# Kernel optimization log

Measured on AMD Instinct MI355X. Metric: run time of the kernel, lower is better.

The kernel has to match this reference:

```python
import jax, jax.numpy as jnp
import numpy as np

BACKBONE_C = 480
NUM_SEG = 4
HIDDEN = 128
IN_DIM = 2 + BACKBONE_C + NUM_SEG + 2  # 488
N_NODES = 200000
N_EDGES = 800000
FH = FW = 128


def _bilinear_sample(feat, vertices, image_size):
    # feat: (C, H, W); vertices: (N, 2) in pixel space.
    # Matches F.grid_sample(..., mode='bilinear', align_corners=True) with
    # grid = vertices/image_size*2 - 1  =>  ix = vx/image_size*(W-1).
    C, H, W = feat.shape
    ix = vertices[:, 0] / image_size * (W - 1)
    iy = vertices[:, 1] / image_size * (H - 1)
    x0 = jnp.floor(ix)
    y0 = jnp.floor(iy)
    wx = ix - x0
    wy = iy - y0
    x0i = jnp.clip(x0.astype(jnp.int32), 0, W - 1)
    x1i = jnp.clip(x0i + 1, 0, W - 1)
    y0i = jnp.clip(y0.astype(jnp.int32), 0, H - 1)
    y1i = jnp.clip(y0i + 1, 0, H - 1)
    f00 = feat[:, y0i, x0i]  # (C, N)
    f01 = feat[:, y0i, x1i]
    f10 = feat[:, y1i, x0i]
    f11 = feat[:, y1i, x1i]
    out = (f00 * (1 - wx) * (1 - wy) + f01 * wx * (1 - wy)
           + f10 * (1 - wx) * wy + f11 * wx * wy)
    return out.T  # (N, C)


def setup_inputs() -> dict:
    key = jax.random.key(0)
    k = jax.random.split(key, 8)
    vertices = jax.random.uniform(k[0], (N_NODES, 2), jnp.float32) * 512.0
    backbone_features = jax.random.normal(k[1], (1, BACKBONE_C, FH, FW), jnp.float32)
    seg_probs = jax.random.uniform(k[2], (1, NUM_SEG, FH, FW), jnp.float32)
    edge_index = jax.random.randint(k[3], (2, N_EDGES), 0, N_NODES, jnp.int64)
    s1 = 1.0 / np.sqrt(IN_DIM)
    s2 = 1.0 / np.sqrt(HIDDEN)
    W1 = jax.random.uniform(k[4], (HIDDEN, IN_DIM), jnp.float32, -s1, s1)
    b1 = jax.random.uniform(k[5], (HIDDEN,), jnp.float32, -s1, s1)
    W2 = jax.random.uniform(k[6], (HIDDEN, HIDDEN), jnp.float32, -s2, s2)
    b2 = jax.random.uniform(k[7], (HIDDEN,), jnp.float32, -s2, s2)
    return {"vertices": vertices, "backbone_features": backbone_features,
            "seg_probs": seg_probs, "edge_index": edge_index,
            "W1": W1, "b1": b1, "W2": W2, "b2": b2, "image_size": 512}


def reference(vertices, backbone_features, seg_probs, edge_index, W1, b1, W2, b2, image_size):
    N = vertices.shape[0]
    coords_norm = vertices / image_size  # (N, 2)
    backbone_feats = _bilinear_sample(backbone_features[0], vertices, image_size)  # (N, C)
    seg_stats = _bilinear_sample(seg_probs[0], vertices, image_size)  # (N, num_seg)
    # degree via scatter-add over both endpoints
    idx = jnp.concatenate([edge_index[0], edge_index[1]]).astype(jnp.int32)
    degree = jax.ops.segment_sum(jnp.ones(idx.shape[0], jnp.float32), idx, num_segments=N)
    degree_norm = degree / (degree.max() + 1e-6)
    # distance to nearest image boundary, normalized by image_size/2
    dx = jnp.minimum(vertices[:, 0], image_size - vertices[:, 0])
    dy = jnp.minimum(vertices[:, 1], image_size - vertices[:, 1])
    dist_to_boundary = jnp.minimum(dx, dy) / (image_size / 2)
    structural = jnp.stack([degree_norm, dist_to_boundary], axis=1)  # (N, 2)
    node_feats = jnp.concatenate([coords_norm, backbone_feats, seg_stats, structural], axis=1)  # (N, 488)
    h = jax.nn.relu(node_feats @ W1.T + b1)
    h = jax.nn.relu(h @ W2.T + b2)
    return h
```

## Files before the change

kernel.cpp:

```cpp
#include <hip/hip_runtime.h>

typedef _Float16 half_t;
typedef __attribute__((ext_vector_type(2))) _Float16 halfx2;
typedef __attribute__((ext_vector_type(8))) _Float16 halfx8;
typedef __attribute__((ext_vector_type(4))) float floatx4;

#define N_NODES 200000
#define N_EDGES 800000
#define NPOS    16384
#define KIN     484

#define NSLICE  32
#define NRANGE  8
#define RNODES  25000
#define RWORDS  6250
#define CWORDS  50000
#define SCHUNK  12500

#define WS_DEGPK 0
#define WS_DEG   6400000
#define WS_MAXD  7200000
#define WS_W1C   7200064
#define WS_W2F   7202112
#define WS_W1F   7234880
#define WS_U     7365952

__global__ __launch_bounds__(256) void k0(const float* __restrict__ W1,
                                          const float* __restrict__ W2,
                                          half_t* __restrict__ w2f,
                                          half_t* __restrict__ w1f,
                                          float4* __restrict__ w1c,
                                          unsigned* __restrict__ maxd) {
  const int tid = threadIdx.x, bid = blockIdx.x;
  const int wave = tid >> 6, lane = tid & 63;
  const int l15 = lane & 15, q4 = lane >> 4;

  if (bid == 0) {
    if (tid == 0) *maxd = 0u;
    if (tid < 128) {
      const float* row = W1 + tid * 488;
      w1c[tid] = make_float4(row[0], row[1], row[486], row[487]);
    }
    for (int i = tid; i < 128 * 128; i += 256) {
      int k8   = i & 7;
      int il15 = (i >> 3) & 15;
      int iq4  = (i >> 7) & 3;
      int ks32 = (i >> 9) & 1;
      int hh   = (i >> 10) & 1;
      int t    = i >> 11;
      int row = t * 16 + il15;
      int col = hh * 64 + ks32 * 32 + iq4 * 8 + k8;
      w2f[i] = (half_t)W2[row * 128 + col];
    }
  } else {
    const int t = bid - 1;
    const int j = t * 16 + l15;
    for (int c = 0; c < 4; ++c) {
      int kbi = c * 4 + wave;
      halfx8 h;
      for (int i = 0; i < 8; ++i) {
        int k = kbi * 32 + q4 * 8 + i;
        h[i] = (half_t)((k < KIN) ? W1[j * 488 + 2 + k] : 0.f);
      }
      *(halfx8*)&w1f[(t * 16 + kbi) * 512 + lane * 8] = h;
    }
  }
}

__global__ __launch_bounds__(256) void k1(const float* __restrict__ bb,
                                          const float* __restrict__ seg,
                                          const int* __restrict__ e,
                                          const half_t* __restrict__ w1f,
                                          unsigned* __restrict__ degpk,
                                          half_t* __restrict__ U) {
  __shared__ __align__(16) char sm[25600];

  const int tid = threadIdx.x, bid = blockIdx.x;
  const int wave = tid >> 6, lane = tid & 63;

  if (bid < 256) {
    const int l15 = lane & 15, q4 = lane >> 4;
    const int kk = lane >> 1, ph = lane & 1;
    const int n0 = bid * 64;
    half_t* Ol = (half_t*)sm;
    half_t* Bp = (half_t*)(sm + 17408) + wave * 640;
    const int pbase = n0 + wave * 16 + ph * 8;

    floatx4 acc[8];
    for (int t = 0; t < 8; ++t) acc[t] = (floatx4){0.f, 0.f, 0.f, 0.f};

    for (int kbi = 0; kbi < 16; ++kbi) {
      const int k = kbi * 32 + kk;
      float vals[8];
      if (k < 480) {
        const float* src = bb + (long)k * NPOS + pbase;
        float4 a = *(const float4*)src;
        float4 b4 = *(const float4*)(src + 4);
        vals[0] = a.x; vals[1] = a.y; vals[2] = a.z; vals[3] = a.w;
        vals[4] = b4.x; vals[5] = b4.y; vals[6] = b4.z; vals[7] = b4.w;
      } else if (k < KIN) {
        const float* src = seg + (long)(k - 480) * NPOS + pbase;
        float4 a = *(const float4*)src;
        float4 b4 = *(const float4*)(src + 4);
        vals[0] = a.x; vals[1] = a.y; vals[2] = a.z; vals[3] = a.w;
        vals[4] = b4.x; vals[5] = b4.y; vals[6] = b4.z; vals[7] = b4.w;
      } else {
        for (int i = 0; i < 8; ++i) vals[i] = 0.f;
      }
      for (int i = 0; i < 8; ++i)
        Bp[(ph * 8 + i) * 40 + kk] = (half_t)vals[i];

      halfx8 af = *(const halfx8*)&Bp[l15 * 40 + q4 * 8];
      for (int t = 0; t < 8; ++t) {
        halfx8 bf = *(const halfx8*)&w1f[(t * 16 + kbi) * 512 + lane * 8];
        acc[t] = __builtin_amdgcn_mfma_f32_16x16x32_f16(af, bf, acc[t], 0, 0, 0);
      }
    }

    for (int t = 0; t < 8; ++t)
      for (int r = 0; r < 4; ++r)
        Ol[(wave * 16 + q4 * 4 + r) * 136 + t * 16 + l15] = (half_t)acc[t][r];
    __syncthreads();
    for (int it = 0; it < 4; ++it) {
      int idx = tid + it * 256;
      int n = idx >> 4, c8 = (idx & 15) * 8;
      *(halfx8*)(U + (long)(n0 + n) * 128 + c8) = *(const halfx8*)&Ol[n * 136 + c8];
    }
  } else {
    unsigned* cnt = (unsigned*)sm;
    const int hb = bid - 256;
    const int s  = hb >> 3;
    const int r  = hb & 7;
    const int lo = r * RNODES;

    for (int i = tid; i < 64 + RWORDS; i += 256) cnt[i] = 0;
    __syncthreads();

#define HBIN(v) { unsigned d = (unsigned)(v) - (unsigned)lo;                 \
                  bool ok = d < (unsigned)RNODES;                            \
                  unsigned w = ok ? (d >> 2) + 64u : (unsigned)lane;         \
                  unsigned a_ = ok ? (1u << ((d & 3u) << 3)) : 0u;           \
                  atomicAdd(&cnt[w], a_); }

    const int4* E4 = (const int4*)e + s * SCHUNK;
    for (int base = 0; base < 12288; base += 1024) {
      int4 a = E4[base + tid];
      int4 b = E4[base + tid + 256];
      int4 c = E4[base + tid + 512];
      int4 d4 = E4[base + tid + 768];
      HBIN(a.x); HBIN(a.y); HBIN(a.z); HBIN(a.w);
      HBIN(b.x); HBIN(b.y); HBIN(b.z); HBIN(b.w);
      HBIN(c.x); HBIN(c.y); HBIN(c.z); HBIN(c.w);
      HBIN(d4.x); HBIN(d4.y); HBIN(d4.z); HBIN(d4.w);
    }
    if (tid < SCHUNK - 12288) {
      int4 a = E4[12288 + tid];
      HBIN(a.x); HBIN(a.y); HBIN(a.z); HBIN(a.w);
    }
#undef HBIN
    __syncthreads();

    unsigned* dst = degpk + s * CWORDS + r * RWORDS;
    for (int i = tid; i < RWORDS; i += 256) dst[i] = cnt[64 + i];
  }
}

__global__ __launch_bounds__(256) void k2(const unsigned* __restrict__ degpk,
                                          unsigned* __restrict__ deg,
                                          unsigned* __restrict__ maxd) {
  const int w4 = blockIdx.x * 256 + threadIdx.x;
  unsigned m = 0;
  if (w4 < CWORDS / 4) {
    uint4 s = make_uint4(0u, 0u, 0u, 0u);
    for (int c = 0; c < NSLICE; ++c) {
      uint4 v = *(const uint4*)&degpk[c * CWORDS + w4 * 4];
      s.x += v.x; s.y += v.y; s.z += v.z; s.w += v.w;
    }
    unsigned words[4] = {s.x, s.y, s.z, s.w};
    for (int k = 0; k < 4; ++k) {
      unsigned sw = words[k];
      uint4 o = make_uint4(sw & 255u, (sw >> 8) & 255u,
                           (sw >> 16) & 255u, sw >> 24);
      *(uint4*)&deg[w4 * 16 + k * 4] = o;
      m = max(m, max(max(o.x, o.y), max(o.z, o.w)));
    }
  }
  for (int off = 32; off > 0; off >>= 1) {
    unsigned o = (unsigned)__shfl_down((int)m, off);
    m = max(m, o);
  }
  if ((threadIdx.x & 63) == 0) atomicMax(maxd, m);
}

__global__ __launch_bounds__(256, 8) void k_main(const float* __restrict__ vertices,
                                              const float4* __restrict__ w1c,
                                              const float* __restrict__ b1,
                                              const float* __restrict__ b2,
                                              const unsigned* __restrict__ deg,
                                              const unsigned* __restrict__ maxd,
                                              const half_t* __restrict__ U,
                                              const half_t* __restrict__ w2f,
                                              float* __restrict__ out) {
  __shared__ half_t At[64 * 136];
  __shared__ int   pPos[64];
  __shared__ float pW[4][64];
  __shared__ float pE[4][64];
  __shared__ float b2l[128];

  const int tid = threadIdx.x;
  const int nodeBase = blockIdx.x * 64;

  if (tid < 128) b2l[tid] = b2[tid];

  if (tid < 64) {
    int n = nodeBase + tid;
    float vx = vertices[2 * n], vy = vertices[2 * n + 1];
    float ix = vx * (127.0f / 512.0f), iy = vy * (127.0f / 512.0f);
    float fx = floorf(ix), fy = floorf(iy);
    float wx = ix - fx, wy = iy - fy;
    int x0 = min(max((int)fx, 0), 127);
    int y0 = min(max((int)fy, 0), 127);
    pPos[tid] = y0 * 128 + x0;
    pW[0][tid] = (1.f - wx) * (1.f - wy);
    pW[1][tid] = wx * (1.f - wy);
    pW[2][tid] = (1.f - wx) * wy;
    pW[3][tid] = wx * wy;
    pE[0][tid] = vx * (1.f / 512.f);
    pE[1][tid] = vy * (1.f / 512.f);
    float md = (float)(*maxd) + 1e-6f;
    pE[2][tid] = (float)deg[n] / md;
    float dx = fminf(vx, 512.f - vx), dy = fminf(vy, 512.f - vy);
    pE[3][tid] = fminf(dx, dy) * (1.f / 256.f);
  }

  const int jp = tid & 63, q = tid >> 6;
  const int j2 = jp * 2;
  float4 cA = w1c[j2], cB = w1c[j2 + 1];
  float c00 = cA.x, c01 = cA.y, c06 = cA.z, c07 = cA.w;
  float c10 = cB.x, c11 = cB.y, c16 = cB.z, c17 = cB.w;
  float bb0 = b1[j2], bb1 = b1[j2 + 1];
  __syncthreads();

#pragma unroll 4
  for (int it = 0; it < 16; ++it) {
    int ln = it * 4 + q;
    int pos = pPos[ln];
    float w00 = pW[0][ln], w01 = pW[1][ln], w10 = pW[2][ln], w11 = pW[3][ln];
    float cx = pE[0][ln], cy = pE[1][ln], dn = pE[2][ln], db = pE[3][ln];
    const half_t* base = U + (long)pos * 128 + j2;
    halfx2 u00 = *(const halfx2*)(base);
    halfx2 u01 = *(const halfx2*)(base + 128);
    halfx2 u10 = *(const halfx2*)(base + 16384);
    halfx2 u11 = *(const halfx2*)(base + 16512);
    float z0 = bb0 + c00 * cx + c01 * cy + c06 * dn + c07 * db
             + w00 * (float)u00.x + w01 * (float)u01.x
             + w10 * (float)u10.x + w11 * (float)u11.x;
    float z1 = bb1 + c10 * cx + c11 * cy + c16 * dn + c17 * db
             + w00 * (float)u00.y + w01 * (float)u01.y
             + w10 * (float)u10.y + w11 * (float)u11.y;
    halfx2 h;
    h.x = (half_t)fmaxf(z0, 0.f);
    h.y = (half_t)fmaxf(z1, 0.f);
    *(halfx2*)&At[ln * 136 + j2] = h;
  }
  __syncthreads();

  const int wave = tid >> 6, lane = tid & 63;
  const int l15 = lane & 15, q4 = lane >> 4;
  const half_t* wf = w2f + (q4 * 16 + l15) * 8;
  floatx4 acc[8];
  for (int t = 0; t < 8; ++t) acc[t] = (floatx4){0.f, 0.f, 0.f, 0.f};

  for (int h = 0; h < 2; ++h)
    for (int ks32 = 0; ks32 < 2; ++ks32) {
      halfx8 af = *(const halfx8*)&At[(wave * 16 + l15) * 136 + h * 64 +
                                      ks32 * 32 + q4 * 8];
      for (int t = 0; t < 8; ++t) {
        halfx8 bf = *(const halfx8*)&wf[(t * 4 + h * 2 + ks32) * 512];
        acc[t] = __builtin_amdgcn_mfma_f32_16x16x32_f16(af, bf, acc[t], 0, 0, 0);
      }
    }

  for (int t = 0; t < 8; ++t) {
    int col = t * 16 + l15;
    float bias = b2l[col];
    int row0 = nodeBase + wave * 16 + q4 * 4;
    for (int r = 0; r < 4; ++r)
      out[(long)(row0 + r) * 128 + col] = fmaxf(acc[t][r] + bias, 0.f);
  }
}

extern "C" void kernel_launch(void* const* d_in, const int* in_sizes, int n_in,
                              void* d_out, int out_size, void* d_ws, size_t ws_size,
                              hipStream_t stream) {
  const float* vertices = (const float*)d_in[0];
  const float* bb       = (const float*)d_in[1];
  const float* seg      = (const float*)d_in[2];
  const int*   edges    = (const int*)d_in[3];
  const float* W1       = (const float*)d_in[4];
  const float* b1       = (const float*)d_in[5];
  const float* W2       = (const float*)d_in[6];
  const float* b2       = (const float*)d_in[7];

  char* ws = (char*)d_ws;
  unsigned* degpk = (unsigned*)(ws + WS_DEGPK);
  unsigned* deg   = (unsigned*)(ws + WS_DEG);
  unsigned* maxd  = (unsigned*)(ws + WS_MAXD);
  float4*   w1c   = (float4*)(ws + WS_W1C);
  half_t*   w2f   = (half_t*)(ws + WS_W2F);
  half_t*   w1f   = (half_t*)(ws + WS_W1F);
  half_t*   U     = (half_t*)(ws + WS_U);
  float*    outp  = (float*)d_out;

  k0<<<9, 256, 0, stream>>>(W1, W2, w2f, w1f, w1c, maxd);
  k1<<<512, 256, 0, stream>>>(bb, seg, edges, w1f, degpk, U);
  k2<<<49, 256, 0, stream>>>(degpk, deg, maxd);
  k_main<<<3125, 256, 0, stream>>>(vertices, w1c, b1, b2, deg, maxd, U, w2f, outp);
}
```

Measured before the change: 209.0 us.

## Fold degree reduction into k1 via grid counter and prefetch GEMM inputs

Removes the separate k2 launch. Histogram blocks in k1 signal completion through an atomic counter, and the first 49 of them spin until all 256 histogram blocks finish before reducing the packed degrees and computing the max. The change also software-pipelines the backbone-feature loads in the k1 GEMM path by prefetching the next k-block into registers. The spin-wait assumes all histogram blocks are co-resident or get scheduled, which risks deadlock or stalls, and the prefetch raises register pressure.

```diff
diff --git a/kernel.cpp b/kernel.cpp
--- a/kernel.cpp
+++ b/kernel.cpp
@@ -36,7 +36,7 @@
   const int l15 = lane & 15, q4 = lane >> 4;
 
   if (bid == 0) {
-    if (tid == 0) *maxd = 0u;
+    if (tid == 0) { maxd[0] = 0u; maxd[1] = 0u; }
     if (tid < 128) {
       const float* row = W1 + tid * 488;
       w1c[tid] = make_float4(row[0], row[1], row[486], row[487]);
@@ -72,6 +72,8 @@
                                           const int* __restrict__ e,
                                           const half_t* __restrict__ w1f,
                                           unsigned* __restrict__ degpk,
+                                          unsigned* __restrict__ deg,
+                                          unsigned* __restrict__ maxd,
                                           half_t* __restrict__ U) {
   __shared__ __align__(16) char sm[25600];
 
@@ -89,33 +91,42 @@
     floatx4 acc[8];
     for (int t = 0; t < 8; ++t) acc[t] = (floatx4){0.f, 0.f, 0.f, 0.f};
 
+#define LOADV(kbi_, dst_) {                                                  \
+      const int k_ = (kbi_) * 32 + kk;                                       \
+      if (k_ < 480) {                                                        \
+        const float* src_ = bb + (long)k_ * NPOS + pbase;                    \
+        float4 a_ = *(const float4*)src_;                                    \
+        float4 b_ = *(const float4*)(src_ + 4);                              \
+        dst_[0] = a_.x; dst_[1] = a_.y; dst_[2] = a_.z; dst_[3] = a_.w;      \
+        dst_[4] = b_.x; dst_[5] = b_.y; dst_[6] = b_.z; dst_[7] = b_.w;      \
+      } else if (k_ < KIN) {                                                 \
+        const float* src_ = seg + (long)(k_ - 480) * NPOS + pbase;           \
+        float4 a_ = *(const float4*)src_;                                    \
+        float4 b_ = *(const float4*)(src_ + 4);                              \
+        dst_[0] = a_.x; dst_[1] = a_.y; dst_[2] = a_.z; dst_[3] = a_.w;      \
+        dst_[4] = b_.x; dst_[5] = b_.y; dst_[6] = b_.z; dst_[7] = b_.w;      \
+      } else {                                                               \
+        for (int i_ = 0; i_ < 8; ++i_) dst_[i_] = 0.f;                       \
+      } }
+
+    float cur[8], nxt[8];
+    LOADV(0, cur);
     for (int kbi = 0; kbi < 16; ++kbi) {
-      const int k = kbi * 32 + kk;
-      float vals[8];
-      if (k < 480) {
-        const float* src = bb + (long)k * NPOS + pbase;
-        float4 a = *(const float4*)src;
-        float4 b4 = *(const float4*)(src + 4);
-        vals[0] = a.x; vals[1] = a.y; vals[2] = a.z; vals[3] = a.w;
-        vals[4] = b4.x; vals[5] = b4.y; vals[6] = b4.z; vals[7] = b4.w;
-      } else if (k < KIN) {
-        const float* src = seg + (long)(k - 480) * NPOS + pbase;
-        float4 a = *(const float4*)src;
-        float4 b4 = *(const float4*)(src + 4);
-        vals[0] = a.x; vals[1] = a.y; vals[2] = a.z; vals[3] = a.w;
-        vals[4] = b4.x; vals[5] = b4.y; vals[6] = b4.z; vals[7] = b4.w;
-      } else {
-        for (int i = 0; i < 8; ++i) vals[i] = 0.f;
-      }
+      if (kbi < 15) LOADV(kbi + 1, nxt);
+#pragma unroll
       for (int i = 0; i < 8; ++i)
-        Bp[(ph * 8 + i) * 40 + kk] = (half_t)vals[i];
+        Bp[(ph * 8 + i) * 40 + kk] = (half_t)cur[i];
 
       halfx8 af = *(const halfx8*)&Bp[l15 * 40 + q4 * 8];
+#pragma unroll
       for (int t = 0; t < 8; ++t) {
         halfx8 bf = *(const halfx8*)&w1f[(t * 16 + kbi) * 512 + lane * 8];
         acc[t] = __builtin_amdgcn_mfma_f32_16x16x32_f16(af, bf, acc[t], 0, 0, 0);
       }
-    }
+#pragma unroll
+      for (int i = 0; i < 8; ++i) cur[i] = nxt[i];
+    }
+#undef LOADV
 
     for (int t = 0; t < 8; ++t)
       for (int r = 0; r < 4; ++r)
@@ -162,34 +173,42 @@
 
     unsigned* dst = degpk + s * CWORDS + r * RWORDS;
     for (int i = tid; i < RWORDS; i += 256) dst[i] = cnt[64 + i];
-  }
-}
-
-__global__ __launch_bounds__(256) void k2(const unsigned* __restrict__ degpk,
-                                          unsigned* __restrict__ deg,
-                                          unsigned* __restrict__ maxd) {
-  const int w4 = blockIdx.x * 256 + threadIdx.x;
-  unsigned m = 0;
-  if (w4 < CWORDS / 4) {
-    uint4 s = make_uint4(0u, 0u, 0u, 0u);
-    for (int c = 0; c < NSLICE; ++c) {
-      uint4 v = *(const uint4*)&degpk[c * CWORDS + w4 * 4];
-      s.x += v.x; s.y += v.y; s.z += v.z; s.w += v.w;
-    }
-    unsigned words[4] = {s.x, s.y, s.z, s.w};
-    for (int k = 0; k < 4; ++k) {
-      unsigned sw = words[k];
-      uint4 o = make_uint4(sw & 255u, (sw >> 8) & 255u,
-                           (sw >> 16) & 255u, sw >> 24);
-      *(uint4*)&deg[w4 * 16 + k * 4] = o;
-      m = max(m, max(max(o.x, o.y), max(o.z, o.w)));
-    }
-  }
-  for (int off = 32; off > 0; off >>= 1) {
-    unsigned o = (unsigned)__shfl_down((int)m, off);
-    m = max(m, o);
-  }
-  if ((threadIdx.x & 63) == 0) atomicMax(maxd, m);
+
+    __threadfence();
+    __syncthreads();
+    if (tid == 0) atomicAdd(&maxd[1], 1u);
+
+    if (hb < 49) {
+      if (tid == 0)
+        while (atomicAdd(&maxd[1], 0u) < (unsigned)(NSLICE * NRANGE))
+          __builtin_amdgcn_s_sleep(8);
+      __syncthreads();
+      __threadfence();
+
+      const int w4 = hb * 256 + tid;
+      unsigned m = 0;
+      if (w4 < CWORDS / 4) {
+        uint4 ssum = make_uint4(0u, 0u, 0u, 0u);
+        for (int c = 0; c < NSLICE; ++c) {
+          uint4 v = *(const uint4*)&degpk[c * CWORDS + w4 * 4];
+          ssum.x += v.x; ssum.y += v.y; ssum.z += v.z; ssum.w += v.w;
+        }
+        unsigned words[4] = {ssum.x, ssum.y, ssum.z, ssum.w};
+        for (int k = 0; k < 4; ++k) {
+          unsigned sw = words[k];
+          uint4 o = make_uint4(sw & 255u, (sw >> 8) & 255u,
+                               (sw >> 16) & 255u, sw >> 24);
+          *(uint4*)&deg[w4 * 16 + k * 4] = o;
+          m = max(m, max(max(o.x, o.y), max(o.z, o.w)));
+        }
+      }
+      for (int off = 32; off > 0; off >>= 1) {
+        unsigned o = (unsigned)__shfl_down((int)m, off);
+        m = max(m, o);
+      }
+      if ((tid & 63) == 0) atomicMax(&maxd[0], m);
+    }
+  }
 }
 
 __global__ __launch_bounds__(256, 8) void k_main(const float* __restrict__ vertices,
@@ -227,7 +246,7 @@
     pW[3][tid] = wx * wy;
     pE[0][tid] = vx * (1.f / 512.f);
     pE[1][tid] = vy * (1.f / 512.f);
-    float md = (float)(*maxd) + 1e-6f;
+    float md = (float)(maxd[0]) + 1e-6f;
     pE[2][tid] = (float)deg[n] / md;
     float dx = fminf(vx, 512.f - vx), dy = fminf(vy, 512.f - vy);
     pE[3][tid] = fminf(dx, dy) * (1.f / 256.f);
@@ -313,7 +332,6 @@
   float*    outp  = (float*)d_out;
 
   k0<<<9, 256, 0, stream>>>(W1, W2, w2f, w1f, w1c, maxd);
-  k1<<<512, 256, 0, stream>>>(bb, seg, edges, w1f, degpk, U);
-  k2<<<49, 256, 0, stream>>>(degpk, deg, maxd);
+  k1<<<512, 256, 0, stream>>>(bb, seg, edges, w1f, degpk, deg, maxd, U);
   k_main<<<3125, 256, 0, stream>>>(vertices, w1c, b1, b2, deg, maxd, U, w2f, outp);
 }
```

Measured after the change: 261.2 us. 1.25x slower.
